# Kernel optimization log

Measured on AMD Instinct MI355X. Metric: run time of the kernel, lower is better.

## Reference

```python
import jax, jax.numpy as jnp
import numpy as np

B, D, H = 131072, 8, 128


def setup_inputs() -> dict:
    key = jax.random.key(0)
    ks = jax.random.split(key, 8)
    s1 = 1.0 / np.sqrt(D + 1)
    s2 = 1.0 / np.sqrt(H)
    return {
        "z": jax.random.normal(ks[0], (B, D), dtype=jnp.float32),
        "logp_z": jnp.zeros((B, 1), dtype=jnp.float32),
        "t": jax.random.uniform(ks[1], (1,), dtype=jnp.float32),
        "W1": jax.random.normal(ks[2], (D + 1, H), dtype=jnp.float32) * s1,
        "b1": jnp.zeros((H,), dtype=jnp.float32),
        "W2": jax.random.normal(ks[3], (H, H), dtype=jnp.float32) * s2,
        "b2": jnp.zeros((H,), dtype=jnp.float32),
        "W3": jax.random.normal(ks[4], (H, D), dtype=jnp.float32) * s2,
        "b3": jnp.zeros((D,), dtype=jnp.float32),
    }


def _net_single(z_i, t_scalar, W1, b1, W2, b2, W3, b3):
    # z_i: [D] -> dz/dt: [D]; FFJORD-style MLP on concat([z, t])
    x = jnp.concatenate([z_i, t_scalar[None]])  # [D+1]
    h = jnp.tanh(x @ W1 + b1)
    h = jnp.tanh(h @ W2 + b2)
    return h @ W3 + b3


def reference(z, logp_z, t, W1, b1, W2, b2, W3, b3):
    t_scalar = t.reshape(())

    def f_i(z_i):
        return _net_single(z_i, t_scalar, W1, b1, W2, b2, W3, b3)

    # dz/dt for every sample (batched forward)
    dz_dt = jax.vmap(f_i)(z)  # [B, D]
    # Exact Jacobian trace: fused forward-mode batched Jacobian (replaces the
    # original's D sequential autograd.grad reverse-mode calls)
    jac = jax.vmap(jax.jacfwd(f_i))(z)  # [B, D, D]
    trace = jnp.einsum("bii->b", jac)  # [B]
    dlogp_z_dt = -trace[:, None]  # [B, 1]
    return (dz_dt, dlogp_z_dt)
```

## Files before the change

kernel.cpp:

```cpp
#include <hip/hip_runtime.h>
#include <hip/hip_bf16.h>

#define BATCH 131072
#define PITCH 136

typedef __bf16 bf16x8 __attribute__((ext_vector_type(8)));
typedef float floatx4 __attribute__((ext_vector_type(4)));

__device__ __forceinline__ float fast_tanh(float x) {
    float e = __expf(2.0f * x);
    return 1.0f - 2.0f * __builtin_amdgcn_rcpf(e + 1.0f);
}


__global__ void prep_kernel(const float* __restrict__ W1,
                            const float* __restrict__ W2,
                            const float* __restrict__ W3,
                            __bf16* __restrict__ ws) {
    int idx = blockIdx.x * 256 + threadIdx.x;
    if (idx < 16384) {
        int j = idx & 7, q = (idx >> 3) & 3, n = (idx >> 5) & 127, kb = idx >> 12;
        int k = kb * 32 + q * 8 + j;
        ws[idx] = (__bf16)W2[k * 128 + n];
        float c = 0.0f;
        #pragma unroll
        for (int d = 0; d < 8; ++d) c += W3[k * 8 + d] * W1[d * 128 + n];
        ws[16384 + idx] = (__bf16)(W2[n * 128 + k] * c);
    } else if (idx < 20480) {
        int t = idx - 16384;
        int j = t & 7, q = (t >> 3) & 3, n = t >> 5;
        int k = q * 8 + j;
        ws[32768 + t] = (k < 9) ? (__bf16)W1[k * 128 + n] : (__bf16)0.0f;
    } else if (idx < 22528) {
        int t = idx - 20480;
        int j = t & 7, q = (t >> 3) & 3, n = (t >> 5) & 15, kb = t >> 9;
        int k = kb * 32 + q * 8 + j;
        ws[36864 + t] = (n < 8) ? (__bf16)W3[k * 8 + n] : (__bf16)0.0f;
    }
}

__global__ __launch_bounds__(256, 2) void cnf_main(
        const float* __restrict__ z, const float* __restrict__ t_ptr,
        const float* __restrict__ b1g, const float* __restrict__ b2g,
        const float* __restrict__ b3g, const __bf16* __restrict__ ws,
        float* __restrict__ out) {
    __shared__ __bf16 sW2s[16384];
    __shared__ __bf16 sW1s[4096];
    __shared__ float sb1[128];
    __shared__ float sb2[128];
    __shared__ __bf16 tile[4][16 * PITCH];

    const int tid = threadIdx.x;
    {
        uint4* dst = (uint4*)sW2s;
        const uint4* src = (const uint4*)ws;
        for (int i = tid; i < 2048; i += 256) dst[i] = src[i];
        uint4* dst1 = (uint4*)sW1s;
        const uint4* src1 = (const uint4*)(ws + 32768);
        for (int i = tid; i < 512; i += 256) dst1[i] = src1[i];
        if (tid < 128) { sb1[tid] = b1g[tid]; sb2[tid] = b2g[tid]; }
    }
    __syncthreads();

    const int lane = tid & 63;
    const int w = tid >> 6;
    const int p = lane & 15;
    const int q = lane >> 4;
    __bf16* T = tile[w];
    const float tval = t_ptr[0];
    const float b3v = (p < 8) ? b3g[p] : 0.0f;
    const bf16x8* W2sv = (const bf16x8*)sW2s;
    const bf16x8* W1sv = (const bf16x8*)sW1s;
    const bf16x8* GTv  = (const bf16x8*)(ws + 16384);
    const bf16x8* W3v  = (const bf16x8*)(ws + 36864);

    for (int it = 0; it < 4; ++it) {
        const int s0 = blockIdx.x * 256 + it * 64 + w * 16;

        bf16x8 ax;
        #pragma unroll
        for (int j = 0; j < 8; ++j) ax[j] = (__bf16)0.0f;
        if (q == 0) {
            const float4 z0 = ((const float4*)(z + (size_t)(s0 + p) * 8))[0];
            const float4 z1 = ((const float4*)(z + (size_t)(s0 + p) * 8))[1];
            ax[0] = (__bf16)z0.x; ax[1] = (__bf16)z0.y;
            ax[2] = (__bf16)z0.z; ax[3] = (__bf16)z0.w;
            ax[4] = (__bf16)z1.x; ax[5] = (__bf16)z1.y;
            ax[6] = (__bf16)z1.z; ax[7] = (__bf16)z1.w;
        } else if (q == 1) {
            ax[0] = (__bf16)tval;
        }

        float a1c[32];
        #pragma unroll
        for (int nt = 0; nt < 8; ++nt) {
            const int n = nt * 16 + p;
            floatx4 acc = {0.f, 0.f, 0.f, 0.f};
            acc = __builtin_amdgcn_mfma_f32_16x16x32_bf16(ax, W1sv[n * 4 + q], acc, 0, 0, 0);
            const float bn = sb1[n];
            #pragma unroll
            for (int r = 0; r < 4; ++r) {
                const float h1 = fast_tanh(acc[r] + bn);
                a1c[nt * 4 + r] = __builtin_fmaf(-h1, h1, 1.0f);
                T[(q * 4 + r) * PITCH + n] = (__bf16)h1;
            }
        }
        bf16x8 ah[4];
        #pragma unroll
        for (int kb = 0; kb < 4; ++kb)
            ah[kb] = *(const bf16x8*)&T[p * PITCH + kb * 32 + q * 8];

        float h2c[32];
        #pragma unroll
        for (int nt = 0; nt < 8; ++nt) {
            const int n = nt * 16 + p;
            floatx4 acc = {0.f, 0.f, 0.f, 0.f};
            #pragma unroll
            for (int kb = 0; kb < 4; ++kb)
                acc = __builtin_amdgcn_mfma_f32_16x16x32_bf16(
                        ah[kb], W2sv[(kb * 128 + n) * 4 + q], acc, 0, 0, 0);
            const float bn = sb2[n];
            #pragma unroll
            for (int r = 0; r < 4; ++r) {
                const float h2 = fast_tanh(acc[r] + bn);
                h2c[nt * 4 + r] = h2;
                const float a2 = __builtin_fmaf(-h2, h2, 1.0f);
                T[(q * 4 + r) * PITCH + n] = (__bf16)a2;
            }
        }
        bf16x8 aa[4];
        #pragma unroll
        for (int kb = 0; kb < 4; ++kb)
            aa[kb] = *(const bf16x8*)&T[p * PITCH + kb * 32 + q * 8];

        float tr[4] = {0.f, 0.f, 0.f, 0.f};
        #pragma unroll
        for (int nt = 0; nt < 8; ++nt) {
            const int n = nt * 16 + p;
            floatx4 acc = {0.f, 0.f, 0.f, 0.f};
            #pragma unroll
            for (int kb = 0; kb < 4; ++kb)
                acc = __builtin_amdgcn_mfma_f32_16x16x32_bf16(
                        aa[kb], GTv[(kb * 128 + n) * 4 + q], acc, 0, 0, 0);
            #pragma unroll
            for (int r = 0; r < 4; ++r)
                tr[r] = __builtin_fmaf(a1c[nt * 4 + r], acc[r], tr[r]);
        }

        #pragma unroll
        for (int i = 0; i < 32; ++i)
            T[(q * 4 + (i & 3)) * PITCH + (i >> 2) * 16 + p] = (__bf16)h2c[i];
        bf16x8 ah2[4];
        #pragma unroll
        for (int kb = 0; kb < 4; ++kb)
            ah2[kb] = *(const bf16x8*)&T[p * PITCH + kb * 32 + q * 8];

        floatx4 acc3 = {0.f, 0.f, 0.f, 0.f};
        #pragma unroll
        for (int kb = 0; kb < 4; ++kb)
            acc3 = __builtin_amdgcn_mfma_f32_16x16x32_bf16(
                    ah2[kb], W3v[(kb * 16 + p) * 4 + q], acc3, 0, 0, 0);
        if (p < 8) {
            #pragma unroll
            for (int r = 0; r < 4; ++r)
                out[(size_t)(s0 + q * 4 + r) * 8 + p] = acc3[r] + b3v;
        }

        #pragma unroll
        for (int r = 0; r < 4; ++r) {
            float v = tr[r];
            v += __shfl_xor(v, 1, 64);
            v += __shfl_xor(v, 2, 64);
            v += __shfl_xor(v, 4, 64);
            v += __shfl_xor(v, 8, 64);
            tr[r] = v;
        }
        if (p == 0) {
            #pragma unroll
            for (int r = 0; r < 4; ++r)
                out[(size_t)BATCH * 8 + s0 + q * 4 + r] = -tr[r];
        }
    }
}

extern "C" void kernel_launch(void* const* d_in, const int* in_sizes, int n_in,
                              void* d_out, int out_size, void* d_ws, size_t ws_size,
                              hipStream_t stream) {
    const float* z  = (const float*)d_in[0];
    const float* t  = (const float*)d_in[2];
    const float* W1 = (const float*)d_in[3];
    const float* b1 = (const float*)d_in[4];
    const float* W2 = (const float*)d_in[5];
    const float* b2 = (const float*)d_in[6];
    const float* W3 = (const float*)d_in[7];
    const float* b3 = (const float*)d_in[8];
    __bf16* ws = (__bf16*)d_ws;
    float* out = (float*)d_out;

    prep_kernel<<<88, 256, 0, stream>>>(W1, W2, W3, ws);
    cnf_main<<<512, 256, 0, stream>>>(z, t, b1, b2, b3, ws, out);
}
```

Measured before the change: 104.0 us.

## Rewrite CNF kernel with transposed fp16 MFMA keeping activations in registers

Rewrites the main kernel in a transposed formulation: weights become the A operand and activations the B operand of 16x16x16 fp16 MFMAs. Each layer's output fragment can then feed the next layer directly from registers, with no LDS tile round-trips. Biases and the tanh exponent scale are folded into the prepacked weights through an augmented ones row, which removes bias adds and multiplies. W1 and W3 fragments now live in registers. Occupancy rises to 4 blocks per CU with 1024 blocks of 128 samples each, and the trace reduction and output stores are simplified. Switching from bf16 to fp16 trades exponent range for mantissa precision, and using more, smaller MFMAs may lower matrix throughput per instruction.

```diff
diff --git a/kernel.cpp b/kernel.cpp
--- a/kernel.cpp
+++ b/kernel.cpp
@@ -1,64 +1,64 @@
 #include <hip/hip_runtime.h>
-#include <hip/hip_bf16.h>
 
 #define BATCH 131072
-#define PITCH 136
-
-typedef __bf16 bf16x8 __attribute__((ext_vector_type(8)));
+#define SC 2.885390081777927f
+
+typedef _Float16 half4 __attribute__((ext_vector_type(4)));
 typedef float floatx4 __attribute__((ext_vector_type(4)));
 
-__device__ __forceinline__ float fast_tanh(float x) {
-    float e = __expf(2.0f * x);
-    return 1.0f - 2.0f * __builtin_amdgcn_rcpf(e + 1.0f);
+__device__ __forceinline__ half4 u2h(uint2 u) { return __builtin_bit_cast(half4, u); }
+
+
+__global__ void prep_kernel(const float* __restrict__ W1, const float* __restrict__ b1,
+                            const float* __restrict__ W2, const float* __restrict__ b2,
+                            const float* __restrict__ W3, const float* __restrict__ b3,
+                            _Float16* __restrict__ ws) {
+    int idx = blockIdx.x * 256 + threadIdx.x;
+    if (idx < 18432) {
+        int j = idx & 3, hf = (idx >> 2) & 1, lane = (idx >> 3) & 63;
+        int rem = idx >> 9, kb = rem % 9, ntp = rem / 9;
+        int m = (2 * ntp + hf) * 16 + (lane & 15);
+        int k = kb * 16 + (lane >> 4) * 4 + j;
+        float v = (k < 128) ? SC * W2[k * 128 + m] : ((k == 128) ? SC * b2[m] : 0.0f);
+        ws[idx] = (_Float16)v;
+    } else if (idx < 34816) {
+        int e = idx - 18432;
+        int j = e & 3, hf = (e >> 2) & 1, lane = (e >> 3) & 63;
+        int rem = e >> 9, kb = rem & 7, ntp = rem >> 3;
+        int h = (2 * ntp + hf) * 16 + (lane & 15);
+        int g = kb * 16 + (lane >> 4) * 4 + j;
+        float c = 0.0f;
+        #pragma unroll
+        for (int d = 0; d < 8; ++d) c += W3[g * 8 + d] * W1[d * 128 + h];
+        ws[idx] = (_Float16)(W2[h * 128 + g] * c);
+    } else if (idx < 36864) {
+        int e = idx - 34816;
+        int j = e & 3, lane = (e >> 2) & 63, nt = e >> 8;
+        int h = nt * 16 + (lane & 15);
+        int k = (lane >> 4) * 4 + j;
+        float v = (k < 9) ? SC * W1[k * 128 + h] : ((k == 9) ? SC * b1[h] : 0.0f);
+        ws[idx] = (_Float16)v;
+    } else if (idx < 39168) {
+        int e = idx - 36864;
+        int j = e & 3, lane = (e >> 2) & 63, kb = e >> 8;
+        int m = lane & 15, k = kb * 16 + (lane >> 4) * 4 + j;
+        float v = 0.0f;
+        if (m < 8) v = (k < 128) ? W3[k * 8 + m] : ((k == 128) ? b3[m] : 0.0f);
+        ws[idx] = (_Float16)v;
+    }
 }
 
-
-__global__ void prep_kernel(const float* __restrict__ W1,
-                            const float* __restrict__ W2,
-                            const float* __restrict__ W3,
-                            __bf16* __restrict__ ws) {
-    int idx = blockIdx.x * 256 + threadIdx.x;
-    if (idx < 16384) {
-        int j = idx & 7, q = (idx >> 3) & 3, n = (idx >> 5) & 127, kb = idx >> 12;
-        int k = kb * 32 + q * 8 + j;
-        ws[idx] = (__bf16)W2[k * 128 + n];
-        float c = 0.0f;
-        #pragma unroll
-        for (int d = 0; d < 8; ++d) c += W3[k * 8 + d] * W1[d * 128 + n];
-        ws[16384 + idx] = (__bf16)(W2[n * 128 + k] * c);
-    } else if (idx < 20480) {
-        int t = idx - 16384;
-        int j = t & 7, q = (t >> 3) & 3, n = t >> 5;
-        int k = q * 8 + j;
-        ws[32768 + t] = (k < 9) ? (__bf16)W1[k * 128 + n] : (__bf16)0.0f;
-    } else if (idx < 22528) {
-        int t = idx - 20480;
-        int j = t & 7, q = (t >> 3) & 3, n = (t >> 5) & 15, kb = t >> 9;
-        int k = kb * 32 + q * 8 + j;
-        ws[36864 + t] = (n < 8) ? (__bf16)W3[k * 8 + n] : (__bf16)0.0f;
-    }
-}
-
-__global__ __launch_bounds__(256, 2) void cnf_main(
+__global__ __launch_bounds__(256, 4) void cnf_main(
         const float* __restrict__ z, const float* __restrict__ t_ptr,
-        const float* __restrict__ b1g, const float* __restrict__ b2g,
-        const float* __restrict__ b3g, const __bf16* __restrict__ ws,
-        float* __restrict__ out) {
-    __shared__ __bf16 sW2s[16384];
-    __shared__ __bf16 sW1s[4096];
-    __shared__ float sb1[128];
-    __shared__ float sb2[128];
-    __shared__ __bf16 tile[4][16 * PITCH];
+        const _Float16* __restrict__ ws, float* __restrict__ out) {
+    __shared__ unsigned short sW2[18432];
 
     const int tid = threadIdx.x;
     {
-        uint4* dst = (uint4*)sW2s;
         const uint4* src = (const uint4*)ws;
-        for (int i = tid; i < 2048; i += 256) dst[i] = src[i];
-        uint4* dst1 = (uint4*)sW1s;
-        const uint4* src1 = (const uint4*)(ws + 32768);
-        for (int i = tid; i < 512; i += 256) dst1[i] = src1[i];
-        if (tid < 128) { sb1[tid] = b1g[tid]; sb2[tid] = b2g[tid]; }
+        uint4* dst = (uint4*)sW2;
+        #pragma unroll
+        for (int i = 0; i < 9; ++i) dst[tid + i * 256] = src[tid + i * 256];
     }
     __syncthreads();
 
@@ -66,120 +66,118 @@
     const int w = tid >> 6;
     const int p = lane & 15;
     const int q = lane >> 4;
-    __bf16* T = tile[w];
+
+    half4 W1f[8], W3f[9];
+    {
+        const uint2* w1a = (const uint2*)(ws + 34816);
+        #pragma unroll
+        for (int nt = 0; nt < 8; ++nt) W1f[nt] = u2h(w1a[nt * 64 + lane]);
+        const uint2* w3a = (const uint2*)(ws + 36864);
+        #pragma unroll
+        for (int kb = 0; kb < 9; ++kb) W3f[kb] = u2h(w3a[kb * 64 + lane]);
+    }
+    half4 e1 = {(_Float16)0.0f, (_Float16)0.0f, (_Float16)0.0f, (_Float16)0.0f};
+    if (q == 0) e1[0] = (_Float16)1.0f;
     const float tval = t_ptr[0];
-    const float b3v = (p < 8) ? b3g[p] : 0.0f;
-    const bf16x8* W2sv = (const bf16x8*)sW2s;
-    const bf16x8* W1sv = (const bf16x8*)sW1s;
-    const bf16x8* GTv  = (const bf16x8*)(ws + 16384);
-    const bf16x8* W3v  = (const bf16x8*)(ws + 36864);
-
-    for (int it = 0; it < 4; ++it) {
-        const int s0 = blockIdx.x * 256 + it * 64 + w * 16;
-
-        bf16x8 ax;
-        #pragma unroll
-        for (int j = 0; j < 8; ++j) ax[j] = (__bf16)0.0f;
-        if (q == 0) {
-            const float4 z0 = ((const float4*)(z + (size_t)(s0 + p) * 8))[0];
-            const float4 z1 = ((const float4*)(z + (size_t)(s0 + p) * 8))[1];
-            ax[0] = (__bf16)z0.x; ax[1] = (__bf16)z0.y;
-            ax[2] = (__bf16)z0.z; ax[3] = (__bf16)z0.w;
-            ax[4] = (__bf16)z1.x; ax[5] = (__bf16)z1.y;
-            ax[6] = (__bf16)z1.z; ax[7] = (__bf16)z1.w;
-        } else if (q == 1) {
-            ax[0] = (__bf16)tval;
-        }
-
-        float a1c[32];
+    const uint4* sW2v = (const uint4*)sW2;
+    const uint4* gav = (const uint4*)(ws + 18432);
+
+    #pragma unroll
+    for (int it = 0; it < 2; ++it) {
+        const int s0 = blockIdx.x * 128 + w * 32 + it * 16;
+
+        const float4 zv = *(const float4*)(z + (size_t)(s0 + p) * 8 + (q & 1) * 4);
+        half4 xb;
+        if (q < 2) {
+            xb[0] = (_Float16)zv.x; xb[1] = (_Float16)zv.y;
+            xb[2] = (_Float16)zv.z; xb[3] = (_Float16)zv.w;
+        } else if (q == 2) {
+            xb[0] = (_Float16)tval; xb[1] = (_Float16)1.0f;
+            xb[2] = (_Float16)0.0f; xb[3] = (_Float16)0.0f;
+        } else {
+            xb[0] = (_Float16)0.0f; xb[1] = (_Float16)0.0f;
+            xb[2] = (_Float16)0.0f; xb[3] = (_Float16)0.0f;
+        }
+
+        half4 h1f[8], a1f[8];
         #pragma unroll
         for (int nt = 0; nt < 8; ++nt) {
-            const int n = nt * 16 + p;
-            floatx4 acc = {0.f, 0.f, 0.f, 0.f};
-            acc = __builtin_amdgcn_mfma_f32_16x16x32_bf16(ax, W1sv[n * 4 + q], acc, 0, 0, 0);
-            const float bn = sb1[n];
+            floatx4 a0 = {0.f, 0.f, 0.f, 0.f};
+            a0 = __builtin_amdgcn_mfma_f32_16x16x16f16(W1f[nt], xb, a0, 0, 0, 0);
             #pragma unroll
             for (int r = 0; r < 4; ++r) {
-                const float h1 = fast_tanh(acc[r] + bn);
-                a1c[nt * 4 + r] = __builtin_fmaf(-h1, h1, 1.0f);
-                T[(q * 4 + r) * PITCH + n] = (__bf16)h1;
-            }
-        }
-        bf16x8 ah[4];
-        #pragma unroll
-        for (int kb = 0; kb < 4; ++kb)
-            ah[kb] = *(const bf16x8*)&T[p * PITCH + kb * 32 + q * 8];
-
-        float h2c[32];
+                const float e = __builtin_amdgcn_exp2f(a0[r]);
+                const float rr = __builtin_amdgcn_rcpf(e + 1.0f);
+                const float h = __builtin_fmaf(-2.0f, rr, 1.0f);
+                h1f[nt][r] = (_Float16)h;
+                a1f[nt][r] = (_Float16)__builtin_fmaf(-h, h, 1.0f);
+            }
+        }
+
+        floatx4 acc[8];
+        #pragma unroll
+        for (int nt = 0; nt < 8; ++nt) acc[nt] = (floatx4){0.f, 0.f, 0.f, 0.f};
+        #pragma unroll
+        for (int kb = 0; kb < 9; ++kb) {
+            const half4 bfrag = (kb < 8) ? h1f[kb] : e1;
+            #pragma unroll
+            for (int ntp = 0; ntp < 4; ++ntp) {
+                const uint4 af = sW2v[(ntp * 9 + kb) * 64 + lane];
+                acc[2 * ntp] = __builtin_amdgcn_mfma_f32_16x16x16f16(
+                        u2h((uint2){af.x, af.y}), bfrag, acc[2 * ntp], 0, 0, 0);
+                acc[2 * ntp + 1] = __builtin_amdgcn_mfma_f32_16x16x16f16(
+                        u2h((uint2){af.z, af.w}), bfrag, acc[2 * ntp + 1], 0, 0, 0);
+            }
+        }
+
+        half4 h2f[8], a2f[8];
         #pragma unroll
         for (int nt = 0; nt < 8; ++nt) {
-            const int n = nt * 16 + p;
-            floatx4 acc = {0.f, 0.f, 0.f, 0.f};
-            #pragma unroll
-            for (int kb = 0; kb < 4; ++kb)
-                acc = __builtin_amdgcn_mfma_f32_16x16x32_bf16(
-                        ah[kb], W2sv[(kb * 128 + n) * 4 + q], acc, 0, 0, 0);
-            const float bn = sb2[n];
             #pragma unroll
             for (int r = 0; r < 4; ++r) {
-                const float h2 = fast_tanh(acc[r] + bn);
-                h2c[nt * 4 + r] = h2;
-                const float a2 = __builtin_fmaf(-h2, h2, 1.0f);
-                T[(q * 4 + r) * PITCH + n] = (__bf16)a2;
-            }
-        }
-        bf16x8 aa[4];
-        #pragma unroll
-        for (int kb = 0; kb < 4; ++kb)
-            aa[kb] = *(const bf16x8*)&T[p * PITCH + kb * 32 + q * 8];
-
-        float tr[4] = {0.f, 0.f, 0.f, 0.f};
+                const float e = __builtin_amdgcn_exp2f(acc[nt][r]);
+                const float rr = __builtin_amdgcn_rcpf(e + 1.0f);
+                const float h = __builtin_fmaf(-2.0f, rr, 1.0f);
+                h2f[nt][r] = (_Float16)h;
+                a2f[nt][r] = (_Float16)__builtin_fmaf(-h, h, 1.0f);
+            }
+        }
+
+        floatx4 acc3 = {0.f, 0.f, 0.f, 0.f};
+        #pragma unroll
+        for (int kb = 0; kb < 9; ++kb)
+            acc3 = __builtin_amdgcn_mfma_f32_16x16x16f16(
+                    W3f[kb], (kb < 8) ? h2f[kb] : e1, acc3, 0, 0, 0);
+        if (q < 2) {
+            float4 o; o.x = acc3[0]; o.y = acc3[1]; o.z = acc3[2]; o.w = acc3[3];
+            *(float4*)(out + (size_t)(s0 + p) * 8 + q * 4) = o;
+        }
+
+        floatx4 accU[8];
+        #pragma unroll
+        for (int nt = 0; nt < 8; ++nt) accU[nt] = (floatx4){0.f, 0.f, 0.f, 0.f};
+        #pragma unroll
+        for (int kb = 0; kb < 8; ++kb) {
+            #pragma unroll
+            for (int ntp = 0; ntp < 4; ++ntp) {
+                const uint4 gf = gav[(ntp * 8 + kb) * 64 + lane];
+                accU[2 * ntp] = __builtin_amdgcn_mfma_f32_16x16x16f16(
+                        u2h((uint2){gf.x, gf.y}), a2f[kb], accU[2 * ntp], 0, 0, 0);
+                accU[2 * ntp + 1] = __builtin_amdgcn_mfma_f32_16x16x16f16(
+                        u2h((uint2){gf.z, gf.w}), a2f[kb], accU[2 * ntp + 1], 0, 0, 0);
+            }
+        }
+
+        float tr = 0.0f;
         #pragma unroll
         for (int nt = 0; nt < 8; ++nt) {
-            const int n = nt * 16 + p;
-            floatx4 acc = {0.f, 0.f, 0.f, 0.f};
-            #pragma unroll
-            for (int kb = 0; kb < 4; ++kb)
-                acc = __builtin_amdgcn_mfma_f32_16x16x32_bf16(
-                        aa[kb], GTv[(kb * 128 + n) * 4 + q], acc, 0, 0, 0);
             #pragma unroll
             for (int r = 0; r < 4; ++r)
-                tr[r] = __builtin_fmaf(a1c[nt * 4 + r], acc[r], tr[r]);
-        }
-
-        #pragma unroll
-        for (int i = 0; i < 32; ++i)
-            T[(q * 4 + (i & 3)) * PITCH + (i >> 2) * 16 + p] = (__bf16)h2c[i];
-        bf16x8 ah2[4];
-        #pragma unroll
-        for (int kb = 0; kb < 4; ++kb)
-            ah2[kb] = *(const bf16x8*)&T[p * PITCH + kb * 32 + q * 8];
-
-        floatx4 acc3 = {0.f, 0.f, 0.f, 0.f};
-        #pragma unroll
-        for (int kb = 0; kb < 4; ++kb)
-            acc3 = __builtin_amdgcn_mfma_f32_16x16x32_bf16(
-                    ah2[kb], W3v[(kb * 16 + p) * 4 + q], acc3, 0, 0, 0);
-        if (p < 8) {
-            #pragma unroll
-            for (int r = 0; r < 4; ++r)
-                out[(size_t)(s0 + q * 4 + r) * 8 + p] = acc3[r] + b3v;
-        }
-
-        #pragma unroll
-        for (int r = 0; r < 4; ++r) {
-            float v = tr[r];
-            v += __shfl_xor(v, 1, 64);
-            v += __shfl_xor(v, 2, 64);
-            v += __shfl_xor(v, 4, 64);
-            v += __shfl_xor(v, 8, 64);
-            tr[r] = v;
-        }
-        if (p == 0) {
-            #pragma unroll
-            for (int r = 0; r < 4; ++r)
-                out[(size_t)BATCH * 8 + s0 + q * 4 + r] = -tr[r];
-        }
+                tr = __builtin_fmaf((float)a1f[nt][r], accU[nt][r], tr);
+        }
+        tr += __shfl_xor(tr, 16, 64);
+        tr += __shfl_xor(tr, 32, 64);
+        if (q == 0) out[(size_t)BATCH * 8 + s0 + p] = -tr;
     }
 }
 
@@ -194,9 +192,9 @@
     const float* b2 = (const float*)d_in[6];
     const float* W3 = (const float*)d_in[7];
     const float* b3 = (const float*)d_in[8];
-    __bf16* ws = (__bf16*)d_ws;
+    _Float16* ws = (_Float16*)d_ws;
     float* out = (float*)d_out;
 
-    prep_kernel<<<88, 256, 0, stream>>>(W1, W2, W3, ws);
-    cnf_main<<<512, 256, 0, stream>>>(z, t, b1, b2, b3, ws, out);
+    prep_kernel<<<153, 256, 0, stream>>>(W1, b1, W2, b2, W3, b3, ws);
+    cnf_main<<<1024, 256, 0, stream>>>(z, t, ws, out);
 }
```

New measurement: 124.0 us. +19.2%, slower.
